# Optimization experiments

Hardware: AMD Instinct MI355X
Metric: run time of the kernel (lower is better)

Reference implementation:

```python
import jax, jax.numpy as jnp
import numpy as np
from functools import reduce

N_QUBITS = 12
DIM = 2 ** N_QUBITS  # 4096
BATCH = 512
TWO_PI = 6.283185307179586


def u3_gate(t):
    # Standard U3(theta, phi, lam) single-qubit gate, complex64 2x2.
    th, ph, la = t[0], t[1], t[2]
    c = jnp.cos(th * 0.5).astype(jnp.complex64)
    s = jnp.sin(th * 0.5).astype(jnp.complex64)
    e_la = jnp.exp(1j * la.astype(jnp.complex64))
    e_ph = jnp.exp(1j * ph.astype(jnp.complex64))
    row0 = jnp.stack([c, -e_la * s])
    row1 = jnp.stack([e_ph * s, e_ph * e_la * c])
    return jnp.stack([row0, row1])  # [2,2] complex64


def full_unitary(thetas):
    # Kron product of per-qubit U3 gates -> [2^n, 2^n] complex64,
    # matching U3(*self.thetas) in the original layer.
    gates = [u3_gate(thetas[i]) for i in range(N_QUBITS)]
    return reduce(jnp.kron, gates)


def setup_inputs() -> dict:
    key = jax.random.key(0)
    k1, k2, k3 = jax.random.split(key, 3)
    thetas = jax.random.uniform(k1, (N_QUBITS, 3), dtype=jnp.float32) * TWO_PI
    state_re = jax.random.normal(k2, (BATCH, DIM, 1), dtype=jnp.float32)
    state_im = jax.random.normal(k3, (BATCH, DIM, 1), dtype=jnp.float32)
    return {"thetas": thetas, "state_re": state_re, "state_im": state_im}


def reference(thetas, state_re, state_im):
    U = full_unitary(thetas)                      # [DIM, DIM] complex64
    state = state_re.astype(jnp.complex64) + 1j * state_im.astype(jnp.complex64)
    out = jnp.einsum('ij,bjk->bik', U, state)     # matrix @ inputs, batched
    # Complex output expressed as real/imag concat on last axis: [B, DIM, 2]
    return jnp.concatenate([out.real, out.imag], axis=-1)
```

## Files before the change

### kernel.cpp

```cpp
#include <hip/hip_runtime.h>
#include <math.h>

#define NQ    12
#define DIM   4096
#define BATCH 512

typedef float nt_f2 __attribute__((ext_vector_type(2)));

#define PAD2(i) ((i) + 2 * ((i) >> 4))

#define LEVEL(q, J) do {                                                    \
    const float4 GA = *(const float4*)&g[q][0];                             \
    const float4 GB = *(const float4*)&g[q][4];                             \
    _Pragma("unroll")                                                       \
    for (int p = 0; p < 8; ++p) {                                           \
        const int r0 = ((p >> (J)) << ((J) + 1)) | (p & ((1 << (J)) - 1));  \
        const int r1 = r0 | (1 << (J));                                     \
        const float ar = x[r0].x, ai = x[r0].y;                             \
        const float br = x[r1].x, bi = x[r1].y;                             \
        x[r0].x = GA.x * ar - GA.y * ai + GA.z * br - GA.w * bi;            \
        x[r0].y = GA.x * ai + GA.y * ar + GA.z * bi + GA.w * br;            \
        x[r1].x = GB.x * ar - GB.y * ai + GB.z * br - GB.w * bi;            \
        x[r1].y = GB.x * ai + GB.y * ar + GB.z * bi + GB.w * br;            \
    }                                                                       \
} while (0)

__global__ __launch_bounds__(256) void u3_apply_kernel(
    const float* __restrict__ thetas,
    const float* __restrict__ sre,
    const float* __restrict__ sim_,
    float*       __restrict__ out)
{
    __shared__ __align__(16) float2 L[4608];
    __shared__ __align__(16) float  g[NQ][8];

    const int b = blockIdx.x;
    const int t = threadIdx.x;

    const float4* pre = (const float4*)(sre  + (size_t)b * DIM) + 4 * t;
    const float4* pim = (const float4*)(sim_ + (size_t)b * DIM) + 4 * t;
    float4 vr0 = pre[0], vr1 = pre[1], vr2 = pre[2], vr3 = pre[3];
    float4 vi0 = pim[0], vi1 = pim[1], vi2 = pim[2], vi3 = pim[3];

    if (t < NQ) {
        float th = thetas[t * 3 + 0];
        float ph = thetas[t * 3 + 1];
        float la = thetas[t * 3 + 2];
        float c, s, cl, sl, cp, sp;
        __sincosf(th * 0.5f, &s, &c);
        __sincosf(la, &sl, &cl);
        __sincosf(ph, &sp, &cp);
        g[t][0] = c;        g[t][1] = 0.0f;
        g[t][2] = -cl * s;  g[t][3] = -sl * s;
        g[t][4] = cp * s;   g[t][5] = sp * s;
        g[t][6] = (cp * cl - sp * sl) * c;
        g[t][7] = (sp * cl + cp * sl) * c;
    }
    __syncthreads();

    float2 x[16];
    x[ 0] = make_float2(vr0.x, vi0.x); x[ 1] = make_float2(vr0.y, vi0.y);
    x[ 2] = make_float2(vr0.z, vi0.z); x[ 3] = make_float2(vr0.w, vi0.w);
    x[ 4] = make_float2(vr1.x, vi1.x); x[ 5] = make_float2(vr1.y, vi1.y);
    x[ 6] = make_float2(vr1.z, vi1.z); x[ 7] = make_float2(vr1.w, vi1.w);
    x[ 8] = make_float2(vr2.x, vi2.x); x[ 9] = make_float2(vr2.y, vi2.y);
    x[10] = make_float2(vr2.z, vi2.z); x[11] = make_float2(vr2.w, vi2.w);
    x[12] = make_float2(vr3.x, vi3.x); x[13] = make_float2(vr3.y, vi3.y);
    x[14] = make_float2(vr3.z, vi3.z); x[15] = make_float2(vr3.w, vi3.w);

    LEVEL(11, 0); LEVEL(10, 1); LEVEL(9, 2); LEVEL(8, 3);

#pragma unroll
    for (int k = 0; k < 8; ++k) {
        *(float4*)&L[PAD2((t << 4) | (2 * k))] =
            make_float4(x[2 * k].x, x[2 * k].y, x[2 * k + 1].x, x[2 * k + 1].y);
    }
    __syncthreads();
    {
        const int base = ((t & 0xF0) << 4) | (t & 15);
#pragma unroll
        for (int r = 0; r < 16; ++r) x[r] = L[PAD2(base | (r << 4))];
    }

    LEVEL(7, 0); LEVEL(6, 1); LEVEL(5, 2); LEVEL(4, 3);

    {
        const int base = ((t & 0xF0) << 4) | (t & 15);
#pragma unroll
        for (int r = 0; r < 16; ++r) L[PAD2(base | (r << 4))] = x[r];
    }
    __syncthreads();
#pragma unroll
    for (int r = 0; r < 16; ++r) x[r] = L[PAD2((r << 8) | t)];

    LEVEL(3, 0); LEVEL(2, 1); LEVEL(1, 2); LEVEL(0, 3);

    {
        float2* o2 = (float2*)out + (size_t)b * DIM;
#pragma unroll
        for (int r = 0; r < 16; ++r) {
            nt_f2 v; v.x = x[r].x; v.y = x[r].y;
            __builtin_nontemporal_store(v, (nt_f2*)&o2[(r << 8) | t]);
        }
    }
}

extern "C" void kernel_launch(void* const* d_in, const int* in_sizes, int n_in,
                              void* d_out, int out_size, void* d_ws, size_t ws_size,
                              hipStream_t stream) {
    const float* thetas = (const float*)d_in[0];
    const float* sre    = (const float*)d_in[1];
    const float* sim_   = (const float*)d_in[2];
    float* out = (float*)d_out;

    u3_apply_kernel<<<BATCH, 256, 0, stream>>>(thetas, sre, sim_, out);
}
```

Before: 16.16 us.

## Process two batch elements per block with prefetched loads of the second

Halves the grid to 256 blocks, each handling two batch elements. Both elements' inputs are loaded up front, so the second element's global loads overlap with the first element's butterfly work, and the gate matrix setup is done once per block instead of once per element. Output stores change from nontemporal to regular stores, and an extra barrier is added before LDS reuse. Costs include higher register pressure from holding 32 extra floats, and on a large GPU with 256 CUs there is only one block per CU, which reduces latency hiding across blocks.

```diff
diff --git a/kernel.cpp b/kernel.cpp
--- a/kernel.cpp
+++ b/kernel.cpp
@@ -4,8 +4,7 @@
 #define NQ    12
 #define DIM   4096
 #define BATCH 512
-
-typedef float nt_f2 __attribute__((ext_vector_type(2)));
+#define NBLK  256
 
 #define PAD2(i) ((i) + 2 * ((i) >> 4))
 
@@ -25,7 +24,49 @@
     }                                                                       \
 } while (0)
 
-__global__ __launch_bounds__(256) void u3_apply_kernel(
+#define UNPACK(v0, v1, v2, v3, w0, w1, w2, w3) do {                         \
+    x[ 0] = make_float2(v0.x, w0.x); x[ 1] = make_float2(v0.y, w0.y);       \
+    x[ 2] = make_float2(v0.z, w0.z); x[ 3] = make_float2(v0.w, w0.w);       \
+    x[ 4] = make_float2(v1.x, w1.x); x[ 5] = make_float2(v1.y, w1.y);       \
+    x[ 6] = make_float2(v1.z, w1.z); x[ 7] = make_float2(v1.w, w1.w);       \
+    x[ 8] = make_float2(v2.x, w2.x); x[ 9] = make_float2(v2.y, w2.y);       \
+    x[10] = make_float2(v2.z, w2.z); x[11] = make_float2(v2.w, w2.w);       \
+    x[12] = make_float2(v3.x, w3.x); x[13] = make_float2(v3.y, w3.y);       \
+    x[14] = make_float2(v3.z, w3.z); x[15] = make_float2(v3.w, w3.w);       \
+} while (0)
+
+__device__ __forceinline__ void butterfly12_store(
+    float2 (&x)[16], float2* __restrict__ L,
+    const float (*__restrict__ g)[8], const int t, float2* __restrict__ o2)
+{
+    LEVEL(11, 0); LEVEL(10, 1); LEVEL(9, 2); LEVEL(8, 3);
+
+    __syncthreads();
+#pragma unroll
+    for (int k = 0; k < 8; ++k) {
+        *(float4*)&L[PAD2((t << 4) | (2 * k))] =
+            make_float4(x[2 * k].x, x[2 * k].y, x[2 * k + 1].x, x[2 * k + 1].y);
+    }
+    __syncthreads();
+    const int base1 = ((t & 0xF0) << 4) | (t & 15);
+#pragma unroll
+    for (int r = 0; r < 16; ++r) x[r] = L[PAD2(base1 | (r << 4))];
+
+    LEVEL(7, 0); LEVEL(6, 1); LEVEL(5, 2); LEVEL(4, 3);
+
+#pragma unroll
+    for (int r = 0; r < 16; ++r) L[PAD2(base1 | (r << 4))] = x[r];
+    __syncthreads();
+#pragma unroll
+    for (int r = 0; r < 16; ++r) x[r] = L[PAD2((r << 8) | t)];
+
+    LEVEL(3, 0); LEVEL(2, 1); LEVEL(1, 2); LEVEL(0, 3);
+
+#pragma unroll
+    for (int r = 0; r < 16; ++r) o2[(r << 8) | t] = x[r];
+}
+
+__global__ __launch_bounds__(256) void u3_pipe2_kernel(
     const float* __restrict__ thetas,
     const float* __restrict__ sre,
     const float* __restrict__ sim_,
@@ -34,18 +75,27 @@
     __shared__ __align__(16) float2 L[4608];
     __shared__ __align__(16) float  g[NQ][8];
 
-    const int b = blockIdx.x;
-    const int t = threadIdx.x;
+    const int blk = blockIdx.x;
+    const int t   = threadIdx.x;
+    const size_t e0 = 2 * (size_t)blk, e1 = e0 + 1;
 
-    const float4* pre = (const float4*)(sre  + (size_t)b * DIM) + 4 * t;
-    const float4* pim = (const float4*)(sim_ + (size_t)b * DIM) + 4 * t;
-    float4 vr0 = pre[0], vr1 = pre[1], vr2 = pre[2], vr3 = pre[3];
-    float4 vi0 = pim[0], vi1 = pim[1], vi2 = pim[2], vi3 = pim[3];
+    float th = 0.f, ph = 0.f, la = 0.f;
+    if (t < NQ) {
+        th = thetas[3 * t + 0];
+        ph = thetas[3 * t + 1];
+        la = thetas[3 * t + 2];
+    }
+
+    const float4* pre0 = (const float4*)(sre  + e0 * DIM) + 4 * t;
+    const float4* pim0 = (const float4*)(sim_ + e0 * DIM) + 4 * t;
+    const float4* pre1 = (const float4*)(sre  + e1 * DIM) + 4 * t;
+    const float4* pim1 = (const float4*)(sim_ + e1 * DIM) + 4 * t;
+    float4 a0 = pre0[0], a1 = pre0[1], a2 = pre0[2], a3 = pre0[3];
+    float4 b0 = pim0[0], b1 = pim0[1], b2 = pim0[2], b3 = pim0[3];
+    float4 c0 = pre1[0], c1 = pre1[1], c2 = pre1[2], c3 = pre1[3];
+    float4 d0 = pim1[0], d1 = pim1[1], d2 = pim1[2], d3 = pim1[3];
 
     if (t < NQ) {
-        float th = thetas[t * 3 + 0];
-        float ph = thetas[t * 3 + 1];
-        float la = thetas[t * 3 + 2];
         float c, s, cl, sl, cp, sp;
         __sincosf(th * 0.5f, &s, &c);
         __sincosf(la, &sl, &cl);
@@ -59,50 +109,12 @@
     __syncthreads();
 
     float2 x[16];
-    x[ 0] = make_float2(vr0.x, vi0.x); x[ 1] = make_float2(vr0.y, vi0.y);
-    x[ 2] = make_float2(vr0.z, vi0.z); x[ 3] = make_float2(vr0.w, vi0.w);
-    x[ 4] = make_float2(vr1.x, vi1.x); x[ 5] = make_float2(vr1.y, vi1.y);
-    x[ 6] = make_float2(vr1.z, vi1.z); x[ 7] = make_float2(vr1.w, vi1.w);
-    x[ 8] = make_float2(vr2.x, vi2.x); x[ 9] = make_float2(vr2.y, vi2.y);
-    x[10] = make_float2(vr2.z, vi2.z); x[11] = make_float2(vr2.w, vi2.w);
-    x[12] = make_float2(vr3.x, vi3.x); x[13] = make_float2(vr3.y, vi3.y);
-    x[14] = make_float2(vr3.z, vi3.z); x[15] = make_float2(vr3.w, vi3.w);
 
-    LEVEL(11, 0); LEVEL(10, 1); LEVEL(9, 2); LEVEL(8, 3);
+    UNPACK(a0, a1, a2, a3, b0, b1, b2, b3);
+    butterfly12_store(x, L, g, t, (float2*)out + e0 * DIM);
 
-#pragma unroll
-    for (int k = 0; k < 8; ++k) {
-        *(float4*)&L[PAD2((t << 4) | (2 * k))] =
-            make_float4(x[2 * k].x, x[2 * k].y, x[2 * k + 1].x, x[2 * k + 1].y);
-    }
-    __syncthreads();
-    {
-        const int base = ((t & 0xF0) << 4) | (t & 15);
-#pragma unroll
-        for (int r = 0; r < 16; ++r) x[r] = L[PAD2(base | (r << 4))];
-    }
-
-    LEVEL(7, 0); LEVEL(6, 1); LEVEL(5, 2); LEVEL(4, 3);
-
-    {
-        const int base = ((t & 0xF0) << 4) | (t & 15);
-#pragma unroll
-        for (int r = 0; r < 16; ++r) L[PAD2(base | (r << 4))] = x[r];
-    }
-    __syncthreads();
-#pragma unroll
-    for (int r = 0; r < 16; ++r) x[r] = L[PAD2((r << 8) | t)];
-
-    LEVEL(3, 0); LEVEL(2, 1); LEVEL(1, 2); LEVEL(0, 3);
-
-    {
-        float2* o2 = (float2*)out + (size_t)b * DIM;
-#pragma unroll
-        for (int r = 0; r < 16; ++r) {
-            nt_f2 v; v.x = x[r].x; v.y = x[r].y;
-            __builtin_nontemporal_store(v, (nt_f2*)&o2[(r << 8) | t]);
-        }
-    }
+    UNPACK(c0, c1, c2, c3, d0, d1, d2, d3);
+    butterfly12_store(x, L, g, t, (float2*)out + e1 * DIM);
 }
 
 extern "C" void kernel_launch(void* const* d_in, const int* in_sizes, int n_in,
@@ -113,5 +125,5 @@
     const float* sim_   = (const float*)d_in[2];
     float* out = (float*)d_out;
 
-    u3_apply_kernel<<<BATCH, 256, 0, stream>>>(thetas, sre, sim_, out);
+    u3_pipe2_kernel<<<NBLK, 256, 0, stream>>>(thetas, sre, sim_, out);
 }
```

After: 17.56 us. 8.6% more time.
